# Kernel tuning notes

Measured on AMD Instinct MI355X. Metric: run time of the kernel, lower is better.

The kernel has to match this reference:

```python
import jax, jax.numpy as jnp
import numpy as np

N, NODE_IN, EDGE_IN, H, ROUNDS = 768, 64, 32, 128, 2


def setup_inputs() -> dict:
    key = jax.random.key(0)
    ks = jax.random.split(key, 12)
    node_feats = jax.random.normal(ks[0], (N, NODE_IN), dtype=jnp.float32)
    edge_feats = jax.random.normal(ks[1], (N, N, EDGE_IN), dtype=jnp.float32)
    adj_mask = jax.random.randint(ks[2], (N, N), 0, 2).astype(jnp.float32)
    def lin(k, fan_in, fan_out):
        w = jax.random.normal(k, (fan_in, fan_out), dtype=jnp.float32) / jnp.sqrt(fan_in)
        return w
    return {
        "node_feats": node_feats,
        "edge_feats": edge_feats,
        "adj_mask": adj_mask,
        "Wn": lin(ks[3], NODE_IN, H), "bn": jnp.zeros((H,), jnp.float32),
        "We": lin(ks[4], EDGE_IN, H), "be": jnp.zeros((H,), jnp.float32),
        "Wa": lin(ks[5], 2 * H, H), "ba": jnp.zeros((H,), jnp.float32),
        "Wu": lin(ks[6], 2 * H, H), "bu": jnp.zeros((H,), jnp.float32),
    }


def reference(node_feats, edge_feats, adj_mask, Wn, bn, We, be, Wa, ba, Wu, bu):
    relu = jax.nn.relu
    h = relu(node_feats @ Wn + bn)                      # (N, H)
    e = relu(jnp.einsum('ijf,fk->ijk', edge_feats, We) + be)  # (N, N, H)
    deg = jnp.clip(adj_mask.sum(axis=0), 1.0)[:, None]  # (N, 1) receiver degree
    # Precompute edge contribution to agg_lin once (constant across rounds):
    # concat([sender, e]) @ Wa == sender @ Wa[:H] + e @ Wa[H:]
    e_proj = jnp.einsum('ijh,hk->ijk', e, Wa[H:])       # (N, N, H)
    for _ in range(ROUNDS):
        s_proj = h @ Wa[:H]                              # (N, H) sender part
        msgs = relu(s_proj[:, None, :] + e_proj + ba)    # (N, N, H)
        agg = jnp.einsum('ijk,ij->jk', msgs, adj_mask) / deg  # masked sum over senders i
        h = relu(jnp.concatenate([h, agg], axis=-1) @ Wu + bu)
    graph_emb = h.mean(axis=0)
    return (h, graph_emb)
```

## Files before the change

kernel.cpp:

```cpp
#include <hip/hip_runtime.h>
#include <hip/hip_bf16.h>


typedef __bf16 bf16x8 __attribute__((ext_vector_type(8)));
typedef float f32x4 __attribute__((ext_vector_type(4)));

#define NN 768

static __device__ __forceinline__ unsigned short to_bf16u(float x) {
    return __builtin_bit_cast(unsigned short, (__bf16)x);
}

__global__ __launch_bounds__(256) void k_prep(
                       const float* __restrict__ ef, unsigned short* __restrict__ efT,
                       const float* __restrict__ adj, float* __restrict__ adjT,
                       const float* __restrict__ We, const float* __restrict__ Wa,
                       unsigned short* __restrict__ WeT, unsigned short* __restrict__ Wa2T,
                       const float* __restrict__ nf, const float* __restrict__ Wn,
                       const float* __restrict__ bn, const float* __restrict__ ba,
                       float* __restrict__ h, float* __restrict__ sp) {
    const int b = blockIdx.x, tid = threadIdx.x;
    if (b < 2304) {
        __shared__ unsigned short tile[8 * 1288 + 8];
        const int i0 = (b % 24) * 32, j0 = (b / 24) * 8;
        {
            const int jj = tid >> 5, ff = tid & 31;
#pragma unroll 4
            for (int i = 0; i < 32; ++i) {
                float v = ef[((size_t)(i0 + i) * NN + j0 + jj) * 32 + ff];
                tile[jj * 1288 + i * 40 + ff] = to_bf16u(v);
            }
        }
        __syncthreads();
        const int tp = tid & 31, j = tid >> 5;
        unsigned short* dst = efT + ((size_t)(j0 + j) * NN + i0) * 32;
#pragma unroll
        for (int v = 0; v < 4; ++v) {
            int flat = v * 256 + tp * 8;
            int i = flat >> 5, f = flat & 31;
            bf16x8 val = *reinterpret_cast<const bf16x8*>(&tile[j * 1288 + i * 40 + f]);
            *reinterpret_cast<bf16x8*>(dst + flat) = val;
        }
    } else if (b < 2880) {
        __shared__ float tile[32][33];
        int bb = b - 2304;
        int bx = bb % 24, by = bb / 24;
        int tx = tid & 31, ty = tid >> 5;
#pragma unroll
        for (int yy = 0; yy < 32; yy += 8)
            tile[ty + yy][tx] = adj[(size_t)(by * 32 + ty + yy) * NN + bx * 32 + tx];
        __syncthreads();
#pragma unroll
        for (int yy = 0; yy < 32; yy += 8)
            adjT[(size_t)(bx * 32 + ty + yy) * NN + by * 32 + tx] = tile[tx][ty + yy];
    } else if (b < 2960) {
        int g = (b - 2880) * 256 + tid;
        if (g < 128 * 32) {
            int c = g >> 5, f = g & 31;
            WeT[g] = to_bf16u(We[f * 128 + c]);
        } else {
            int g2 = g - 128 * 32;
            int c = g2 >> 7, k = g2 & 127;
            Wa2T[g2] = to_bf16u(Wa[(128 + k) * 128 + c]);
        }
    } else {
        __shared__ float nf_l[2][64];
        __shared__ float h_l[2][128];
        int row = tid >> 7, t = tid & 127;
        int i = (b - 2960) * 2 + row;
        if (t < 64) nf_l[row][t] = nf[i * 64 + t];
        __syncthreads();
        float acc = bn[t];
#pragma unroll 8
        for (int f = 0; f < 64; ++f) acc += nf_l[row][f] * Wn[f * 128 + t];
        acc = fmaxf(acc, 0.f);
        h[i * 128 + t] = acc;
        h_l[row][t] = acc;
        __syncthreads();
        float spv = ba[t];
#pragma unroll 8
        for (int f = 0; f < 128; ++f) spv += h_l[row][f] * Wa[f * 128 + t];
        sp[i * 128 + t] = spv;
    }
}

__global__ __launch_bounds__(512) void k_big_s(
    const unsigned short* __restrict__ efT, const float* __restrict__ adjT,
    const float* __restrict__ sp, const unsigned short* __restrict__ WeT,
    const unsigned short* __restrict__ Wa2T, const float* __restrict__ be,
    float* __restrict__ agg) {
    __shared__ __align__(16) unsigned short e_lds[2][2][16 * 128];
    __shared__ float adj_lds[NN];
    __shared__ float be_lds[128];
    __shared__ float wred[8];
    __shared__ float s_invdeg;

    const int tid  = threadIdx.x;
    const int j    = blockIdx.x;
    const int lane = tid & 63;
    const int wv   = tid >> 6;
    const int wr   = wv >> 2;
    const int wc   = wv & 3;
    const int lg   = lane >> 4;
    const int lr   = lane & 15;

    float asum = 0.f;
    for (int k = tid; k < NN; k += 512) {
        float a = adjT[(size_t)j * NN + k];
        adj_lds[k] = a;
        asum += a;
    }
#pragma unroll
    for (int off = 32; off; off >>= 1) asum += __shfl_down(asum, off);
    if (lane == 0) wred[wv] = asum;
    if (tid < 128) be_lds[tid] = be[tid];

    bf16x8 bwe[2];
    bf16x8 bwa[2][4];
#pragma unroll
    for (int t = 0; t < 2; ++t) {
        const int col = 32 * wc + 16 * t + lr;
        bwe[t] = *reinterpret_cast<const bf16x8*>(WeT + col * 32 + 8 * lg);
#pragma unroll
        for (int s = 0; s < 4; ++s)
            bwa[t][s] = *reinterpret_cast<const bf16x8*>(Wa2T + col * 128 + 32 * s + 8 * lg);
    }
    __syncthreads();
    if (tid == 0) {
        float d = 0.f;
#pragma unroll
        for (int w = 0; w < 8; ++w) d += wred[w];
        s_invdeg = 1.0f / fmaxf(d, 1.0f);
    }

    float aggp[2] = {0.f, 0.f};

    auto load_ef = [&](int n, bf16x8& x) {
        int row = 32 * n + 16 * wr + lr;
        x = *reinterpret_cast<const bf16x8*>(efT + ((size_t)j * NN + row) * 32 + 8 * lg);
    };
    auto gemm1 = [&](bf16x8 a, int buf) {
#pragma unroll
        for (int t = 0; t < 2; ++t) {
            const int col = 32 * wc + 16 * t + lr;
            float bb = be_lds[col];
            f32x4 c;
            c[0] = bb; c[1] = bb; c[2] = bb; c[3] = bb;
            f32x4 C1 = __builtin_amdgcn_mfma_f32_16x16x32_bf16(a, bwe[t], c, 0, 0, 0);
#pragma unroll
            for (int r = 0; r < 4; ++r) {
                int row = 4 * lg + r;
                int idx = (row * 128 + col) ^ ((row & 7) << 3);
                e_lds[buf][wr][idx] = to_bf16u(fmaxf(C1[r], 0.f));
            }
        }
    };

    bf16x8 cA;
    load_ef(0, cA);
    gemm1(cA, 0);
    load_ef(1, cA);
    __syncthreads();

    for (int n = 0; n < 24; ++n) {
        const int b = n & 1;
        bf16x8 pA;
        if (n + 2 < 24) load_ef(n + 2, pA);
        if (n + 1 < 24) gemm1(cA, b ^ 1);

        bf16x8 ae[4];
#pragma unroll
        for (int s = 0; s < 4; ++s) {
            int idx = (lr * 128 + 32 * s + 8 * lg) ^ ((lr & 7) << 3);
            ae[s] = *reinterpret_cast<const bf16x8*>(&e_lds[b][wr][idx]);
        }
        const int i0 = 32 * n + 16 * wr + 4 * lg;
        f32x4 av = *reinterpret_cast<const f32x4*>(&adj_lds[i0]);
#pragma unroll
        for (int t = 0; t < 2; ++t) {
            const int col = 32 * wc + 16 * t + lr;
            f32x4 acc;
#pragma unroll
            for (int r = 0; r < 4; ++r)
                acc[r] = sp[(size_t)(i0 + r) * 128 + col];
#pragma unroll
            for (int s = 0; s < 4; ++s)
                acc = __builtin_amdgcn_mfma_f32_16x16x32_bf16(ae[s], bwa[t][s], acc, 0, 0, 0);
#pragma unroll
            for (int r = 0; r < 4; ++r)
                aggp[t] += fmaxf(acc[r], 0.f) * av[r];
        }

        if (n + 2 < 24) cA = pA;
        __syncthreads();
    }

    float* red = reinterpret_cast<float*>(&e_lds[0][0][0]);
#pragma unroll
    for (int t = 0; t < 2; ++t) {
        float v = aggp[t];
        v += __shfl_xor(v, 16);
        v += __shfl_xor(v, 32);
        if (lane < 16) red[wv * 32 + 16 * t + lane] = v;
    }
    __syncthreads();
    if (tid < 128) {
        int wcol = tid >> 5, c32 = tid & 31;
        agg[(size_t)j * 128 + tid] =
            (red[wcol * 32 + c32] + red[(4 + wcol) * 32 + c32]) * s_invdeg;
    }
}

template <int LAST>
__global__ __launch_bounds__(256) void k_upd(
                      const float* __restrict__ h_in, const float* __restrict__ agg,
                      const float* __restrict__ Wu, const float* __restrict__ bu,
                      const float* __restrict__ Wa, const float* __restrict__ ba,
                      float* __restrict__ h_out, float* __restrict__ sp,
                      float* __restrict__ out) {
    __shared__ float buf[2][256];
    __shared__ float hn[2][128];
    const int tid = threadIdx.x;
    const int row = tid >> 7, t = tid & 127;
    const int i = blockIdx.x * 2 + row;
    buf[row][t] = h_in[i * 128 + t];
    buf[row][128 + t] = agg[i * 128 + t];
    __syncthreads();
    float acc = bu[t];
#pragma unroll 8
    for (int f = 0; f < 256; ++f) acc += buf[row][f] * Wu[f * 128 + t];
    acc = fmaxf(acc, 0.f);
    if (LAST) {
        out[i * 128 + t] = acc;
    } else {
        h_out[i * 128 + t] = acc;
        hn[row][t] = acc;
        __syncthreads();
        float spv = ba[t];
#pragma unroll 8
        for (int f = 0; f < 128; ++f) spv += hn[row][f] * Wa[f * 128 + t];
        sp[i * 128 + t] = spv;
    }
}

__global__ __launch_bounds__(64) void k_gemb(const float* __restrict__ out_h, float* __restrict__ out) {
    int c = blockIdx.x, l = threadIdx.x;
    float acc = 0.f;
    for (int i = l; i < NN; i += 64) acc += out_h[(size_t)i * 128 + c];
#pragma unroll
    for (int off = 32; off; off >>= 1) acc += __shfl_down(acc, off);
    if (l == 0) out[NN * 128 + c] = acc * (1.0f / 768.0f);
}

extern "C" void kernel_launch(void* const* d_in, const int* in_sizes, int n_in,
                              void* d_out, int out_size, void* d_ws, size_t ws_size,
                              hipStream_t stream) {
    const float* nf  = (const float*)d_in[0];
    const float* ef  = (const float*)d_in[1];
    const float* adj = (const float*)d_in[2];
    const float* Wn  = (const float*)d_in[3];
    const float* bn  = (const float*)d_in[4];
    const float* We  = (const float*)d_in[5];
    const float* be  = (const float*)d_in[6];
    const float* Wa  = (const float*)d_in[7];
    const float* ba  = (const float*)d_in[8];
    const float* Wu  = (const float*)d_in[9];
    const float* bu  = (const float*)d_in[10];
    float* out = (float*)d_out;

    float* h_buf = (float*)d_ws;
    float* agg   = h_buf + NN * 128;
    float* sp    = agg + NN * 128;
    float* adjT  = sp + (NN + 1) * 128;
    unsigned short* WeT  = (unsigned short*)(adjT + NN * NN);
    unsigned short* Wa2T = WeT + 128 * 32;
    unsigned short* efT  = Wa2T + 128 * 128;

    k_prep<<<3344, 256, 0, stream>>>(ef, efT, adj, adjT, We, Wa, WeT, Wa2T,
                                     nf, Wn, bn, ba, h_buf, sp);

    k_big_s<<<NN, 512, 0, stream>>>(efT, adjT, sp, WeT, Wa2T, be, agg);
    k_upd<0><<<NN / 2, 256, 0, stream>>>(h_buf, agg, Wu, bu, Wa, ba, h_buf, sp, out);
    k_big_s<<<NN, 512, 0, stream>>>(efT, adjT, sp, WeT, Wa2T, be, agg);
    k_upd<1><<<NN / 2, 256, 0, stream>>>(h_buf, agg, Wu, bu, Wa, ba, h_buf, sp, out);

    k_gemb<<<128, 64, 0, stream>>>(out, out);
}
```

Measured before the change: 139.8 us.

## Restructure message kernel to per-wave row slabs with Wa2 staged in LDS

The per-receiver message kernel now uses 256 threads, and each wave owns a 192-row slab of senders and all 128 output columns. The old layout was a 2x4 wave grid in which waves shared double-buffered edge tiles. Each wave recomputes its own edge embedding tile into a private LDS buffer, so the per-iteration block barrier goes away. The Wa[H:] weights move from registers to a swizzled 32KB LDS copy, read on every MFMA. This trades block-wide syncs and duplicated weight registers for more LDS traffic and a larger LDS footprint, which may lower occupancy.

```diff
diff --git a/kernel.cpp b/kernel.cpp
--- a/kernel.cpp
+++ b/kernel.cpp
@@ -84,28 +84,36 @@
     }
 }
 
-__global__ __launch_bounds__(512) void k_big_s(
+__global__ __launch_bounds__(256) void k_big_s(
     const unsigned short* __restrict__ efT, const float* __restrict__ adjT,
     const float* __restrict__ sp, const unsigned short* __restrict__ WeT,
     const unsigned short* __restrict__ Wa2T, const float* __restrict__ be,
     float* __restrict__ agg) {
-    __shared__ __align__(16) unsigned short e_lds[2][2][16 * 128];
+    __shared__ unsigned short wa2_lds[128 * 128];
+    __shared__ __align__(16) unsigned short e_lds[4][16 * 128];
     __shared__ float adj_lds[NN];
-    __shared__ float be_lds[128];
-    __shared__ float wred[8];
+    __shared__ float wred[4];
     __shared__ float s_invdeg;
 
     const int tid  = threadIdx.x;
     const int j    = blockIdx.x;
     const int lane = tid & 63;
     const int wv   = tid >> 6;
-    const int wr   = wv >> 2;
-    const int wc   = wv & 3;
     const int lg   = lane >> 4;
     const int lr   = lane & 15;
 
+    {
+        const int col = tid >> 1;
+        const int kb  = (tid & 1) * 64;
+#pragma unroll
+        for (int m = 0; m < 8; ++m) {
+            bf16x8 v = *reinterpret_cast<const bf16x8*>(Wa2T + col * 128 + kb + 8 * m);
+            int idx = (col * 128 + kb + 8 * m) ^ ((col & 7) << 3);
+            *reinterpret_cast<bf16x8*>(&wa2_lds[idx]) = v;
+        }
+    }
     float asum = 0.f;
-    for (int k = tid; k < NN; k += 512) {
+    for (int k = tid; k < NN; k += 256) {
         float a = adjT[(size_t)j * NN + k];
         adj_lds[k] = a;
         asum += a;
@@ -113,101 +121,90 @@
 #pragma unroll
     for (int off = 32; off; off >>= 1) asum += __shfl_down(asum, off);
     if (lane == 0) wred[wv] = asum;
-    if (tid < 128) be_lds[tid] = be[tid];
-
-    bf16x8 bwe[2];
-    bf16x8 bwa[2][4];
-#pragma unroll
-    for (int t = 0; t < 2; ++t) {
-        const int col = 32 * wc + 16 * t + lr;
+
+    bf16x8 bwe[8];
+    float bereg[8];
+#pragma unroll
+    for (int t = 0; t < 8; ++t) {
+        int col = 16 * t + lr;
         bwe[t] = *reinterpret_cast<const bf16x8*>(WeT + col * 32 + 8 * lg);
-#pragma unroll
-        for (int s = 0; s < 4; ++s)
-            bwa[t][s] = *reinterpret_cast<const bf16x8*>(Wa2T + col * 128 + 32 * s + 8 * lg);
-    }
-    __syncthreads();
-    if (tid == 0) {
-        float d = 0.f;
-#pragma unroll
-        for (int w = 0; w < 8; ++w) d += wred[w];
-        s_invdeg = 1.0f / fmaxf(d, 1.0f);
-    }
-
-    float aggp[2] = {0.f, 0.f};
-
-    auto load_ef = [&](int n, bf16x8& x) {
-        int row = 32 * n + 16 * wr + lr;
+        bereg[t] = be[col];
+    }
+    __syncthreads();
+    if (tid == 0) s_invdeg = 1.0f / fmaxf(wred[0] + wred[1] + wred[2] + wred[3], 1.0f);
+
+    float aggp[8] = {0.f, 0.f, 0.f, 0.f, 0.f, 0.f, 0.f, 0.f};
+
+    const int rowbase = 192 * wv;
+    auto load_ef = [&](int c, bf16x8& x) {
+        int row = rowbase + 16 * c + lr;
         x = *reinterpret_cast<const bf16x8*>(efT + ((size_t)j * NN + row) * 32 + 8 * lg);
     };
-    auto gemm1 = [&](bf16x8 a, int buf) {
-#pragma unroll
-        for (int t = 0; t < 2; ++t) {
-            const int col = 32 * wc + 16 * t + lr;
-            float bb = be_lds[col];
-            f32x4 c;
-            c[0] = bb; c[1] = bb; c[2] = bb; c[3] = bb;
-            f32x4 C1 = __builtin_amdgcn_mfma_f32_16x16x32_bf16(a, bwe[t], c, 0, 0, 0);
-#pragma unroll
-            for (int r = 0; r < 4; ++r) {
-                int row = 4 * lg + r;
-                int idx = (row * 128 + col) ^ ((row & 7) << 3);
-                e_lds[buf][wr][idx] = to_bf16u(fmaxf(C1[r], 0.f));
-            }
-        }
-    };
 
     bf16x8 cA;
     load_ef(0, cA);
-    gemm1(cA, 0);
-    load_ef(1, cA);
-    __syncthreads();
-
-    for (int n = 0; n < 24; ++n) {
-        const int b = n & 1;
+
+    for (int c = 0; c < 12; ++c) {
         bf16x8 pA;
-        if (n + 2 < 24) load_ef(n + 2, pA);
-        if (n + 1 < 24) gemm1(cA, b ^ 1);
-
+        if (c + 1 < 12) load_ef(c + 1, pA);
+
+#pragma unroll
+        for (int t = 0; t < 8; ++t) {
+            f32x4 cc;
+            cc[0] = bereg[t]; cc[1] = bereg[t]; cc[2] = bereg[t]; cc[3] = bereg[t];
+            f32x4 C1 = __builtin_amdgcn_mfma_f32_16x16x32_bf16(cA, bwe[t], cc, 0, 0, 0);
+#pragma unroll
+            for (int r = 0; r < 4; ++r) {
+                int row = 4 * lg + r, col = 16 * t + lr;
+                int idx = (row * 128 + col) ^ ((row & 7) << 3);
+                e_lds[wv][idx] = to_bf16u(fmaxf(C1[r], 0.f));
+            }
+        }
         bf16x8 ae[4];
 #pragma unroll
         for (int s = 0; s < 4; ++s) {
             int idx = (lr * 128 + 32 * s + 8 * lg) ^ ((lr & 7) << 3);
-            ae[s] = *reinterpret_cast<const bf16x8*>(&e_lds[b][wr][idx]);
-        }
-        const int i0 = 32 * n + 16 * wr + 4 * lg;
+            ae[s] = *reinterpret_cast<const bf16x8*>(&e_lds[wv][idx]);
+        }
+        const int i0 = rowbase + 16 * c + 4 * lg;
         f32x4 av = *reinterpret_cast<const f32x4*>(&adj_lds[i0]);
 #pragma unroll
-        for (int t = 0; t < 2; ++t) {
-            const int col = 32 * wc + 16 * t + lr;
+        for (int t = 0; t < 8; ++t) {
+            const int col = 16 * t + lr;
             f32x4 acc;
 #pragma unroll
             for (int r = 0; r < 4; ++r)
                 acc[r] = sp[(size_t)(i0 + r) * 128 + col];
 #pragma unroll
-            for (int s = 0; s < 4; ++s)
-                acc = __builtin_amdgcn_mfma_f32_16x16x32_bf16(ae[s], bwa[t][s], acc, 0, 0, 0);
+            for (int s = 0; s < 4; ++s) {
+                int widx = (col * 128 + 32 * s + 8 * lg) ^ ((col & 7) << 3);
+                bf16x8 bw = *reinterpret_cast<const bf16x8*>(&wa2_lds[widx]);
+                acc = __builtin_amdgcn_mfma_f32_16x16x32_bf16(ae[s], bw, acc, 0, 0, 0);
+            }
 #pragma unroll
             for (int r = 0; r < 4; ++r)
                 aggp[t] += fmaxf(acc[r], 0.f) * av[r];
         }
 
-        if (n + 2 < 24) cA = pA;
-        __syncthreads();
-    }
-
-    float* red = reinterpret_cast<float*>(&e_lds[0][0][0]);
-#pragma unroll
-    for (int t = 0; t < 2; ++t) {
+        if (c + 1 < 12) cA = pA;
+    }
+
+    float* redw = reinterpret_cast<float*>(&e_lds[wv][0]);
+    __syncthreads();
+#pragma unroll
+    for (int t = 0; t < 8; ++t) {
         float v = aggp[t];
         v += __shfl_xor(v, 16);
         v += __shfl_xor(v, 32);
-        if (lane < 16) red[wv * 32 + 16 * t + lane] = v;
+        if (lane < 16) redw[16 * t + lane] = v;
     }
     __syncthreads();
     if (tid < 128) {
-        int wcol = tid >> 5, c32 = tid & 31;
-        agg[(size_t)j * 128 + tid] =
-            (red[wcol * 32 + c32] + red[(4 + wcol) * 32 + c32]) * s_invdeg;
+        const float* r0 = reinterpret_cast<const float*>(&e_lds[0][0]);
+        const float* r1 = reinterpret_cast<const float*>(&e_lds[1][0]);
+        const float* r2 = reinterpret_cast<const float*>(&e_lds[2][0]);
+        const float* r3 = reinterpret_cast<const float*>(&e_lds[3][0]);
+        agg[(size_t)j * 128 + tid] = (r0[tid] + r1[tid] + r2[tid] + r3[tid]) * s_invdeg;
     }
 }
 
@@ -271,7 +268,7 @@
     float* h_buf = (float*)d_ws;
     float* agg   = h_buf + NN * 128;
     float* sp    = agg + NN * 128;
-    float* adjT  = sp + (NN + 1) * 128;
+    float* adjT  = sp + NN * 128;
     unsigned short* WeT  = (unsigned short*)(adjT + NN * NN);
     unsigned short* Wa2T = WeT + 128 * 32;
     unsigned short* efT  = Wa2T + 128 * 128;
@@ -279,9 +276,9 @@
     k_prep<<<3344, 256, 0, stream>>>(ef, efT, adj, adjT, We, Wa, WeT, Wa2T,
                                      nf, Wn, bn, ba, h_buf, sp);
 
-    k_big_s<<<NN, 512, 0, stream>>>(efT, adjT, sp, WeT, Wa2T, be, agg);
+    k_big_s<<<NN, 256, 0, stream>>>(efT, adjT, sp, WeT, Wa2T, be, agg);
     k_upd<0><<<NN / 2, 256, 0, stream>>>(h_buf, agg, Wu, bu, Wa, ba, h_buf, sp, out);
-    k_big_s<<<NN, 512, 0, stream>>>(efT, adjT, sp, WeT, Wa2T, be, agg);
+    k_big_s<<<NN, 256, 0, stream>>>(efT, adjT, sp, WeT, Wa2T, be, agg);
     k_upd<1><<<NN / 2, 256, 0, stream>>>(h_buf, agg, Wu, bu, Wa, ba, h_buf, sp, out);
 
     k_gemb<<<128, 64, 0, stream>>>(out, out);
```

Result: slower. 219.3 us (+56.8%).
